# Kernel tuning notes

Measured on AMD Instinct MI355X. Metric: run time of the kernel, lower is better.

The kernel has to match this reference:

```python
import jax, jax.numpy as jnp
import numpy as np

B, N, K = 8, 16384, 64
SIGMA = 0.2
BN_EPS = 1e-5


def setup_inputs() -> dict:
    key = jax.random.key(0)
    k0, k1, k2, k3 = jax.random.split(key, 4)
    normals = jax.random.normal(k0, (B, 3, N), dtype=jnp.float32)
    neighbor_index = jax.random.randint(k1, (B, N, 3), 0, N)
    weight_alpha = jax.random.uniform(k2, (1, K, 4), dtype=jnp.float32) * np.pi
    weight_beta = jax.random.uniform(k3, (1, K, 4), dtype=jnp.float32) * (2.0 * np.pi)
    bn_gamma = jnp.ones((K,), dtype=jnp.float32)
    bn_beta = jnp.zeros((K,), dtype=jnp.float32)
    return {
        "normals": normals,
        "neighbor_index": neighbor_index,
        "weight_alpha": weight_alpha,
        "weight_beta": weight_beta,
        "bn_gamma": bn_gamma,
        "bn_beta": bn_beta,
    }


def reference(normals, neighbor_index, weight_alpha, weight_beta, bn_gamma, bn_beta):
    # normals: [b, 3, n]; neighbor_index: [b, n, 3]
    # gather the 3 neighbor normals per face -> [b, 3, n, 3]
    neighbor = jax.vmap(lambda nm, idx: nm[:, idx])(normals, neighbor_index)
    # fea points: center + 3 neighbors -> [b, 3, n, 4]
    fea = jnp.concatenate([normals[:, :, :, None], neighbor], axis=3)

    # kernel points on unit sphere: [3, K, 4]
    w = jnp.concatenate(
        [
            jnp.sin(weight_alpha) * jnp.cos(weight_beta),
            jnp.sin(weight_alpha) * jnp.sin(weight_beta),
            jnp.cos(weight_alpha),
        ],
        axis=0,
    )

    fn2 = jnp.sum(fea * fea, axis=1)              # [b, n, 4]
    wn2 = jnp.sum(w * w, axis=0)                  # [K, 4]
    dot = jnp.einsum("bcni,ckj->bknij", fea, w)   # [b, K, n, 4, 4]
    dist = fn2[:, None, :, :, None] + wn2[None, :, None, None, :] - 2.0 * dot

    # Gaussian kernel correlation, averaged over the 4x4 point pairs -> [b, K, n]
    kc = jnp.sum(jnp.exp(dist / (-2.0 * SIGMA * SIGMA)), axis=(3, 4)) / 16.0

    # BatchNorm1d (training-mode batch stats, biased variance) + ReLU
    mean = jnp.mean(kc, axis=(0, 2), keepdims=True)
    var = jnp.var(kc, axis=(0, 2), keepdims=True)
    y = bn_gamma[None, :, None] * (kc - mean) / jnp.sqrt(var + BN_EPS) + bn_beta[None, :, None]
    return jax.nn.relu(y)
```

## Files before the change

### kernel.cpp

```cpp
#include <hip/hip_runtime.h>
#include <math.h>


#define NFACES 16384
#define BATCH  8
#define KK     64

__device__ __constant__ const float C_SCALE = -18.033688011112043f;

__global__ __launch_bounds__(256, 8) void kc_kernel(
    const float* __restrict__ normals,
    const int*   __restrict__ nbr,
    const float* __restrict__ walpha,
    const float* __restrict__ wbeta,
    float*       __restrict__ out)
{
    __shared__ float4 sW[KK * 4];

    const int tid = threadIdx.x;

    {
        float a = walpha[tid];
        float b = wbeta[tid];
        float sa = sinf(a), ca = cosf(a);
        float sb = sinf(b), cb = cosf(b);
        float wx = sa * cb, wy = sa * sb, wz = ca;
        float wn2 = wx * wx + wy * wy + wz * wz;
        const float m2 = -2.0f * C_SCALE;
        sW[tid] = make_float4(m2 * wx, m2 * wy, m2 * wz, C_SCALE * wn2);
    }
    __syncthreads();

    const int b  = blockIdx.x >> 8;
    const int n  = ((blockIdx.x & 255) << 6) + (tid & 63);
    const int kq = tid >> 6;

    const float* nb_ = normals + (size_t)b * 3 * NFACES;

    float fx[4], fy[4], fz[4], fa[4];
    fx[0] = nb_[n];
    fy[0] = nb_[NFACES + n];
    fz[0] = nb_[2 * NFACES + n];
    const int* ip = nbr + ((size_t)b * NFACES + n) * 3;
#pragma unroll
    for (int j = 0; j < 3; ++j) {
        int idx = ip[j];
        fx[j + 1] = nb_[idx];
        fy[j + 1] = nb_[NFACES + idx];
        fz[j + 1] = nb_[2 * NFACES + idx];
    }
#pragma unroll
    for (int i = 0; i < 4; ++i)
        fa[i] = C_SCALE * (fx[i] * fx[i] + fy[i] * fy[i] + fz[i] * fz[i]);

    float* outp = out + ((size_t)b * KK + kq * 16) * NFACES + n;
    const float4* wp = &sW[kq * 64];

#pragma unroll 2
    for (int kk = 0; kk < 16; ++kk) {
        float s = 0.0f;
#pragma unroll
        for (int j = 0; j < 4; ++j) {
            float4 w = wp[kk * 4 + j];
#pragma unroll
            for (int i = 0; i < 4; ++i) {
                float t = __builtin_fmaf(w.z, fz[i], w.w);
                t = __builtin_fmaf(w.y, fy[i], t);
                t = __builtin_fmaf(w.x, fx[i], t);
                t += fa[i];
                s += __builtin_amdgcn_exp2f(t);
            }
        }
        outp[(size_t)kk * NFACES] = s * 0.0625f;
    }
}

__global__ __launch_bounds__(256) void sum_kernel(
    const float* __restrict__ out,
    float*       __restrict__ psum,
    float*       __restrict__ psumsq)
{
    const int k = blockIdx.x & 63;
    const int b = blockIdx.x >> 6;
    const float4* p = reinterpret_cast<const float4*>(
        out + ((size_t)b * KK + k) * NFACES);

    float s = 0.0f, q = 0.0f;
#pragma unroll
    for (int i = 0; i < 16; ++i) {
        float4 v = p[i * 256 + threadIdx.x];
        s += (v.x + v.y) + (v.z + v.w);
        q += (v.x * v.x + v.y * v.y) + (v.z * v.z + v.w * v.w);
    }

    __shared__ float sS[4], sQ[4];
#pragma unroll
    for (int off = 32; off > 0; off >>= 1) {
        s += __shfl_down(s, off, 64);
        q += __shfl_down(q, off, 64);
    }
    const int lane = threadIdx.x & 63, wid = threadIdx.x >> 6;
    if (lane == 0) { sS[wid] = s; sQ[wid] = q; }
    __syncthreads();
    if (threadIdx.x == 0) {
        psum[k * 8 + b]   = (sS[0] + sS[1]) + (sS[2] + sS[3]);
        psumsq[k * 8 + b] = (sQ[0] + sQ[1]) + (sQ[2] + sQ[3]);
    }
}

__global__ __launch_bounds__(64) void fin_kernel(
    const float* __restrict__ psum,
    const float* __restrict__ psumsq,
    const float* __restrict__ gamma,
    const float* __restrict__ beta,
    float*       __restrict__ scale,
    float*       __restrict__ shift)
{
    const int k = threadIdx.x;
    float sum = 0.0f, sq = 0.0f;
#pragma unroll
    for (int b = 0; b < 8; ++b) {
        sum += psum[k * 8 + b];
        sq  += psumsq[k * 8 + b];
    }
    const float invN = 1.0f / (float)(BATCH * NFACES);
    float mean = sum * invN;
    float var  = sq * invN - mean * mean;
    float sc = gamma[k] / sqrtf(var + 1e-5f);
    scale[k] = sc;
    shift[k] = beta[k] - mean * sc;
}

__global__ __launch_bounds__(256) void bn_kernel(
    float* __restrict__ out,
    const float* __restrict__ scale,
    const float* __restrict__ shift)
{
    const size_t idx = (size_t)blockIdx.x * 256 + threadIdx.x;
    const int k = (int)((idx >> 12) & 63);
    float4 v = reinterpret_cast<float4*>(out)[idx];
    const float sc = scale[k], sh = shift[k];
    v.x = fmaxf(__builtin_fmaf(v.x, sc, sh), 0.0f);
    v.y = fmaxf(__builtin_fmaf(v.y, sc, sh), 0.0f);
    v.z = fmaxf(__builtin_fmaf(v.z, sc, sh), 0.0f);
    v.w = fmaxf(__builtin_fmaf(v.w, sc, sh), 0.0f);
    reinterpret_cast<float4*>(out)[idx] = v;
}

extern "C" void kernel_launch(void* const* d_in, const int* in_sizes, int n_in,
                              void* d_out, int out_size, void* d_ws, size_t ws_size,
                              hipStream_t stream) {
    const float* normals = (const float*)d_in[0];
    const int*   nbr     = (const int*)d_in[1];
    const float* walpha  = (const float*)d_in[2];
    const float* wbeta   = (const float*)d_in[3];
    const float* gamma   = (const float*)d_in[4];
    const float* beta    = (const float*)d_in[5];
    float* out = (float*)d_out;

    float* psum   = (float*)d_ws;
    float* psumsq = psum + KK * 8;
    float* scale  = psumsq + KK * 8;
    float* shift  = scale + KK;

    kc_kernel<<<BATCH * 256, 256, 0, stream>>>(normals, nbr, walpha, wbeta, out);
    sum_kernel<<<512, 256, 0, stream>>>(out, psum, psumsq);
    fin_kernel<<<1, 64, 0, stream>>>(psum, psumsq, gamma, beta, scale, shift);

    const int total_f4 = (BATCH * KK * NFACES) / 4;
    bn_kernel<<<total_f4 / 256, 256, 0, stream>>>(out, scale, shift);
}
```

Before: 56.78 us.

## Fuse BN statistic partial sums into the correlation kernel and drop sum pass

```diff
diff --git a/kernel.cpp b/kernel.cpp
--- a/kernel.cpp
+++ b/kernel.cpp
@@ -5,17 +5,21 @@
 #define NFACES 16384
 #define BATCH  8
 #define KK     64
+#define NBLK   2048
 
 __device__ __constant__ const float C_SCALE = -18.033688011112043f;
 
-__global__ __launch_bounds__(256, 8) void kc_kernel(
+__global__ __launch_bounds__(256, 7) void kc_kernel(
     const float* __restrict__ normals,
     const int*   __restrict__ nbr,
     const float* __restrict__ walpha,
     const float* __restrict__ wbeta,
-    float*       __restrict__ out)
+    float*       __restrict__ out,
+    float*       __restrict__ psum,
+    float*       __restrict__ psumsq)
 {
     __shared__ float4 sW[KK * 4];
+    __shared__ float  sT[4][64][17];
 
     const int tid = threadIdx.x;
 
@@ -31,9 +35,10 @@
     }
     __syncthreads();
 
-    const int b  = blockIdx.x >> 8;
-    const int n  = ((blockIdx.x & 255) << 6) + (tid & 63);
-    const int kq = tid >> 6;
+    const int b    = blockIdx.x >> 8;
+    const int lane = tid & 63;
+    const int n    = ((blockIdx.x & 255) << 6) + lane;
+    const int kq   = tid >> 6;
 
     const float* nb_ = normals + (size_t)b * 3 * NFACES;
 
@@ -56,7 +61,7 @@
     float* outp = out + ((size_t)b * KK + kq * 16) * NFACES + n;
     const float4* wp = &sW[kq * 64];
 
-#pragma unroll 2
+#pragma unroll 4
     for (int kk = 0; kk < 16; ++kk) {
         float s = 0.0f;
 #pragma unroll
@@ -71,26 +76,50 @@
                 s += __builtin_amdgcn_exp2f(t);
             }
         }
-        outp[(size_t)kk * NFACES] = s * 0.0625f;
+        float kc = s * 0.0625f;
+        outp[(size_t)kk * NFACES] = kc;
+        sT[kq][lane][kk] = kc;
+    }
+
+    {
+        const int kk = lane & 15, seg = lane >> 4;
+        float v = 0.0f, q = 0.0f;
+#pragma unroll
+        for (int j = 0; j < 16; ++j) {
+            float x = sT[kq][seg * 16 + j][kk];
+            v += x;
+            q = __builtin_fmaf(x, x, q);
+        }
+        v += __shfl_xor(v, 16, 64);  q += __shfl_xor(q, 16, 64);
+        v += __shfl_xor(v, 32, 64);  q += __shfl_xor(q, 32, 64);
+        if (seg == 0) {
+            const int k = kq * 16 + kk;
+            psum[(size_t)k * NBLK + blockIdx.x]   = v;
+            psumsq[(size_t)k * NBLK + blockIdx.x] = q;
+        }
     }
 }
 
-__global__ __launch_bounds__(256) void sum_kernel(
-    const float* __restrict__ out,
-    float*       __restrict__ psum,
-    float*       __restrict__ psumsq)
+__global__ __launch_bounds__(256) void fin_kernel(
+    const float* __restrict__ psum,
+    const float* __restrict__ psumsq,
+    const float* __restrict__ gamma,
+    const float* __restrict__ beta,
+    float*       __restrict__ scale,
+    float*       __restrict__ shift)
 {
-    const int k = blockIdx.x & 63;
-    const int b = blockIdx.x >> 6;
-    const float4* p = reinterpret_cast<const float4*>(
-        out + ((size_t)b * KK + k) * NFACES);
+    const int k = blockIdx.x;
+    const int tid = threadIdx.x;
+    const float4* ps = reinterpret_cast<const float4*>(psum   + (size_t)k * NBLK);
+    const float4* pq = reinterpret_cast<const float4*>(psumsq + (size_t)k * NBLK);
 
     float s = 0.0f, q = 0.0f;
 #pragma unroll
-    for (int i = 0; i < 16; ++i) {
-        float4 v = p[i * 256 + threadIdx.x];
-        s += (v.x + v.y) + (v.z + v.w);
-        q += (v.x * v.x + v.y * v.y) + (v.z * v.z + v.w * v.w);
+    for (int i = 0; i < 2; ++i) {
+        float4 a = ps[i * 256 + tid];
+        float4 c = pq[i * 256 + tid];
+        s += (a.x + a.y) + (a.z + a.w);
+        q += (c.x + c.y) + (c.z + c.w);
     }
 
     __shared__ float sS[4], sQ[4];
@@ -99,36 +128,19 @@
         s += __shfl_down(s, off, 64);
         q += __shfl_down(q, off, 64);
     }
-    const int lane = threadIdx.x & 63, wid = threadIdx.x >> 6;
+    const int lane = tid & 63, wid = tid >> 6;
     if (lane == 0) { sS[wid] = s; sQ[wid] = q; }
     __syncthreads();
-    if (threadIdx.x == 0) {
-        psum[k * 8 + b]   = (sS[0] + sS[1]) + (sS[2] + sS[3]);
-        psumsq[k * 8 + b] = (sQ[0] + sQ[1]) + (sQ[2] + sQ[3]);
+    if (tid == 0) {
+        float sum = (sS[0] + sS[1]) + (sS[2] + sS[3]);
+        float sq  = (sQ[0] + sQ[1]) + (sQ[2] + sQ[3]);
+        const float invN = 1.0f / (float)(BATCH * NFACES);
+        float mean = sum * invN;
+        float var  = sq * invN - mean * mean;
+        float sc = gamma[k] / sqrtf(var + 1e-5f);
+        scale[k] = sc;
+        shift[k] = beta[k] - mean * sc;
     }
-}
-
-__global__ __launch_bounds__(64) void fin_kernel(
-    const float* __restrict__ psum,
-    const float* __restrict__ psumsq,
-    const float* __restrict__ gamma,
-    const float* __restrict__ beta,
-    float*       __restrict__ scale,
-    float*       __restrict__ shift)
-{
-    const int k = threadIdx.x;
-    float sum = 0.0f, sq = 0.0f;
-#pragma unroll
-    for (int b = 0; b < 8; ++b) {
-        sum += psum[k * 8 + b];
-        sq  += psumsq[k * 8 + b];
-    }
-    const float invN = 1.0f / (float)(BATCH * NFACES);
-    float mean = sum * invN;
-    float var  = sq * invN - mean * mean;
-    float sc = gamma[k] / sqrtf(var + 1e-5f);
-    scale[k] = sc;
-    shift[k] = beta[k] - mean * sc;
 }
 
 __global__ __launch_bounds__(256) void bn_kernel(
@@ -159,13 +171,12 @@
     float* out = (float*)d_out;
 
     float* psum   = (float*)d_ws;
-    float* psumsq = psum + KK * 8;
-    float* scale  = psumsq + KK * 8;
+    float* psumsq = psum + KK * NBLK;
+    float* scale  = psumsq + KK * NBLK;
     float* shift  = scale + KK;
 
-    kc_kernel<<<BATCH * 256, 256, 0, stream>>>(normals, nbr, walpha, wbeta, out);
-    sum_kernel<<<512, 256, 0, stream>>>(out, psum, psumsq);
-    fin_kernel<<<1, 64, 0, stream>>>(psum, psumsq, gamma, beta, scale, shift);
+    kc_kernel<<<NBLK, 256, 0, stream>>>(normals, nbr, walpha, wbeta, out, psum, psumsq);
+    fin_kernel<<<KK, 256, 0, stream>>>(psum, psumsq, gamma, beta, scale, shift);
 
     const int total_f4 = (BATCH * KK * NFACES) / 4;
     bn_kernel<<<total_f4 / 256, 256, 0, stream>>>(out, scale, shift);
```

After: 54.07 us. -4.8%, faster.
